# Optimization experiments

Measured on AMD Instinct MI355X. Metric: run time of the kernel, lower is better.

The kernel has to match this reference:

```python
import jax, jax.numpy as jnp
import numpy as np

B, T, V, E, U, D1, D2, C = 256, 512, 32000, 100, 512, 1024, 1024, 10
SCALE = 0.02


def setup_inputs() -> dict:
    key = jax.random.key(0)
    ks = jax.random.split(key, 12)
    return {
        "tokens": jax.random.randint(ks[0], (B, T), 0, V, dtype=jnp.int32),
        "emb": jax.random.normal(ks[1], (V, E), jnp.float32) * SCALE,
        "Wx": jax.random.normal(ks[2], (E, U), jnp.float32) * SCALE,
        "Wh": jax.random.normal(ks[3], (U, U), jnp.float32) * SCALE,
        "b_rnn": jnp.zeros((U,), jnp.float32),
        "W1": jax.random.normal(ks[4], (U, D1), jnp.float32) * SCALE,
        "b1": jnp.zeros((D1,), jnp.float32),
        "W2": jax.random.normal(ks[5], (D1, D2), jnp.float32) * SCALE,
        "b2": jnp.zeros((D2,), jnp.float32),
        "Wo": jax.random.normal(ks[6], (D2, C), jnp.float32) * SCALE,
        "bo": jnp.zeros((C,), jnp.float32),
    }


def reference(tokens, emb, Wx, Wh, b_rnn, W1, b1, W2, b2, Wo, bo):
    # Embedding with mask_zero=True: token 0 produces a masked timestep.
    x = emb[tokens]                      # [B, T, E]
    mask = tokens != 0                   # [B, T] bool

    # SimpleRNN (activation=relu, return last state). Masked steps carry state.
    xw = jnp.einsum("bte,eu->btu", x, Wx) + b_rnn  # precompute input projection [B,T,U]

    def step(h, inp):
        xw_t, m_t = inp                  # [B,U], [B]
        h_new = jax.nn.relu(xw_t + h @ Wh)
        h = jnp.where(m_t[:, None], h_new, h)
        return h, None

    h0 = jnp.zeros((tokens.shape[0], Wh.shape[0]), x.dtype)
    h_last, _ = jax.lax.scan(step, h0, (jnp.swapaxes(xw, 0, 1), mask.T))

    # MLP head: relu, relu, softmax
    h = jax.nn.relu(h_last @ W1 + b1)
    h = jax.nn.relu(h @ W2 + b2)
    return jax.nn.softmax(h @ Wo + bo, axis=-1)
```

## Files before the change

### kernel.cpp

```cpp
#include <hip/hip_runtime.h>


typedef __attribute__((ext_vector_type(8))) int i32x8_t;
typedef __attribute__((ext_vector_type(4))) float f32x4_t;

constexpr int Bn = 256, Tn = 512, En = 100, Un = 512;
constexpr int D1n = 1024, D2n = 1024, Cn = 10;
constexpr float QS  = 256.f;
constexpr float INV = 1.52587890625e-05f;
constexpr int USC = 0x7F7F7F7F;
constexpr int XW_STEP = 16 * 512 * 16;

__device__ __forceinline__ unsigned f2e4m3_sw(float x) {
    unsigned u = __float_as_uint(x);
    unsigned sgn = (u >> 24) & 0x80;
    float a = __uint_as_float(u & 0x7FFFFFFF);
    if (a >= 448.f) return sgn | 0x7E;
    if (a < 0.015625f) {
        unsigned q = (unsigned)__float2int_rn(a * 512.f);
        return sgn | q;
    }
    int e = (int)((u >> 23) & 0xFF) - 127;
    unsigned m = u & 0x7FFFFF;
    unsigned mant = m >> 20, rem = m & 0xFFFFF;
    if (rem > 0x80000 || (rem == 0x80000 && (mant & 1))) {
        if (++mant == 8) { mant = 0; ++e; }
    }
    if (e > 8) return sgn | 0x7E;
    return sgn | ((unsigned)(e + 7) << 3) | mant;
}

__device__ __forceinline__ unsigned cvt1(float x) {
#if __has_builtin(__builtin_amdgcn_cvt_pk_fp8_f32)
    return (unsigned)__builtin_amdgcn_cvt_pk_fp8_f32(x, x, 0, false) & 0xFFu;
#else
    return f2e4m3_sw(x);
#endif
}

__device__ __forceinline__ unsigned pk4(float a, float b, float c, float d) {
#if __has_builtin(__builtin_amdgcn_cvt_pk_fp8_f32)
    int r = __builtin_amdgcn_cvt_pk_fp8_f32(a, b, 0, false);
    r = __builtin_amdgcn_cvt_pk_fp8_f32(c, d, r, true);
    return (unsigned)r;
#else
    return f2e4m3_sw(a) | (f2e4m3_sw(b) << 8) | (f2e4m3_sw(c) << 16) |
           (f2e4m3_sw(d) << 24);
#endif
}

__device__ __forceinline__ ushort f2bf(float x) {
    unsigned u = __float_as_uint(x);
    unsigned r = (u + 0x7FFFu + ((u >> 16) & 1u)) >> 16;
    return (ushort)r;
}

__global__ __launch_bounds__(256) void pack_wh8(const float* __restrict__ Wh,
                                                unsigned char* __restrict__ P) {
    int e = blockIdx.x * 256 + threadIdx.x;
    int j = e & 31, l = (e >> 5) & 63, kc = (e >> 11) & 3, nt = e >> 13;
    int k = kc * 128 + (l >> 4) * 32 + j;
    int c = nt * 16 + (l & 15);
    P[e] = (unsigned char)cvt1(Wh[k * Un + c] * QS);
}

__global__ __launch_bounds__(256) void pack_wx8(const float* __restrict__ Wx,
                                                unsigned char* __restrict__ P) {
    int e = blockIdx.x * 256 + threadIdx.x;
    int j = e & 31, l = (e >> 5) & 63, nt = e >> 11;
    int k = (l >> 4) * 32 + j;
    int c = nt * 16 + (l & 15);
    P[e] = (k < En) ? (unsigned char)cvt1(Wx[k * Un + c] * QS) : 0;
}

__global__ __launch_bounds__(512) void xw_gemm(
    const int* __restrict__ tokens, const float* __restrict__ emb,
    const float* __restrict__ b_rnn, const unsigned char* __restrict__ WxP8,
    ushort* __restrict__ xwp)
{
    __shared__ char XS[32768];

    const int tid  = threadIdx.x;
    const int lane = tid & 63;
    const int wv   = tid >> 6;
    const int r0   = blockIdx.x * 16;
    const int t0   = blockIdx.y * 16;

    const int r16 = lane & 15;
    const int q   = lane >> 4;

    for (int idx = tid; idx < 6400; idx += 512) {
        int tt   = idx / 400;
        int rem  = idx - tt * 400;
        int prow = rem / 25;
        int pc4  = rem - prow * 25;
        int tok  = tokens[(r0 + prow) * Tn + t0 + tt];
        float4 v = *(const float4*)(emb + tok * En + pc4 * 4);
        *(unsigned*)(XS + tt * 2048 + ((prow * 128 + pc4 * 4) ^ (prow << 4))) =
            pk4(v.x * QS, v.y * QS, v.z * QS, v.w * QS);
    }
    for (int idx = tid; idx < 16 * 16 * 7; idx += 512) {
        int tt   = idx / 112;
        int rem  = idx - tt * 112;
        int prow = rem / 7;
        int c4   = 25 + (rem - prow * 7);
        *(unsigned*)(XS + tt * 2048 + ((prow * 128 + c4 * 4) ^ (prow << 4))) = 0;
    }
    __syncthreads();

    i32x8_t wxf[4];
#pragma unroll
    for (int p = 0; p < 4; ++p)
        wxf[p] = *(const i32x8_t*)(WxP8 + ((wv * 4 + p) * 64 + lane) * 32);

    float biasQ[4][4];
#pragma unroll
    for (int p = 0; p < 4; ++p)
#pragma unroll
        for (int j = 0; j < 4; ++j)
            biasQ[p][j] = b_rnn[(wv * 4 + p) * 16 + q * 4 + j] * 65536.f;

    const int bswz = r16 << 4;
    for (int tt = 0; tt < 16; ++tt) {
        uint4 blo = *(const uint4*)(XS + tt * 2048 +
                        ((r16 * 128 + q * 32) ^ bswz));
        uint4 bhi = *(const uint4*)(XS + tt * 2048 +
                        (((r16 * 128 + q * 32) + 16) ^ bswz));
        i32x8_t bf = {(int)blo.x, (int)blo.y, (int)blo.z, (int)blo.w,
                      (int)bhi.x, (int)bhi.y, (int)bhi.z, (int)bhi.w};
        f32x4_t acc[4];
#pragma unroll
        for (int p = 0; p < 4; ++p) {
            acc[p] = (f32x4_t){biasQ[p][0], biasQ[p][1], biasQ[p][2], biasQ[p][3]};
            acc[p] = __builtin_amdgcn_mfma_scale_f32_16x16x128_f8f6f4(
                wxf[p], bf, acc[p], 0, 0, 0, USC, 0, USC);
        }
        size_t base = (((size_t)(t0 + tt) * 16 + blockIdx.x) * 512 + tid) * 16;
        uint4 lo, hi;
        lo.x = (unsigned)f2bf(acc[0][0]) | ((unsigned)f2bf(acc[0][1]) << 16);
        lo.y = (unsigned)f2bf(acc[0][2]) | ((unsigned)f2bf(acc[0][3]) << 16);
        lo.z = (unsigned)f2bf(acc[1][0]) | ((unsigned)f2bf(acc[1][1]) << 16);
        lo.w = (unsigned)f2bf(acc[1][2]) | ((unsigned)f2bf(acc[1][3]) << 16);
        hi.x = (unsigned)f2bf(acc[2][0]) | ((unsigned)f2bf(acc[2][1]) << 16);
        hi.y = (unsigned)f2bf(acc[2][2]) | ((unsigned)f2bf(acc[2][3]) << 16);
        hi.z = (unsigned)f2bf(acc[3][0]) | ((unsigned)f2bf(acc[3][1]) << 16);
        hi.w = (unsigned)f2bf(acc[3][2]) | ((unsigned)f2bf(acc[3][3]) << 16);
        *(uint4*)(xwp + base)     = lo;
        *(uint4*)(xwp + base + 8) = hi;
    }
}

__global__ __launch_bounds__(512, 2) void rnn_persist8x(
    const int* __restrict__ tokens, const unsigned char* __restrict__ WhP8,
    const ushort* __restrict__ xwp, float* __restrict__ h_final)
{
    __shared__ char sh[32768];
    char* H0 = sh;            char* H1 = sh + 8192;
    char* TOKB = sh + 16384;

    const int tid  = threadIdx.x;
    const int lane = tid & 63;
    const int wv   = tid >> 6;
    const int r0   = blockIdx.x * 16;

    const int r16  = lane & 15;
    const int q    = lane >> 4;
    const int bswz = r16 << 4;

    for (int f = tid; f < 16 * Tn; f += 512) {
        int row = f >> 9, tt = f & 511;
        *(ushort*)(TOKB + ((((row << 10) | (tt << 1))) ^ (row << 2))) =
            (ushort)tokens[r0 * Tn + f];
    }
    {
        int* z = (int*)sh;
        for (int f = tid; f < 2048; f += 512) z[f] = 0;
    }
    __syncthreads();

    i32x8_t whf[4][4];
#pragma unroll
    for (int kc = 0; kc < 4; ++kc)
#pragma unroll
        for (int p = 0; p < 4; ++p)
            whf[kc][p] = *(const i32x8_t*)(WhP8 +
                (((wv * 4 + p) * 4 + kc) * 64 + lane) * 32);

    const ushort* xwT = xwp + ((size_t)blockIdx.x * 512 + tid) * 16;

    float hprev[4][4];
#pragma unroll
    for (int p = 0; p < 4; ++p)
#pragma unroll
        for (int j = 0; j < 4; ++j) hprev[p][j] = 0.f;

    uint4 pfA0, pfA1, pfB0, pfB1;
    pfA0 = *(const uint4*)(xwT);
    pfA1 = *(const uint4*)(xwT + 8);

#define BFL(u) __uint_as_float((u) << 16)
#define BFH(u) __uint_as_float((u) & 0xFFFF0000u)

#define RNN_STEP(T, HC, HN, C0, C1, N0, N1)                                    \
    {                                                                          \
        const int t = (T);                                                     \
        if (t + 1 < Tn) {                                                      \
            const ushort* xt = xwT + (size_t)(t + 1) * XW_STEP;                \
            N0 = *(const uint4*)(xt);                                          \
            N1 = *(const uint4*)(xt + 8);                                      \
        }                                                                      \
        f32x4_t acc[4];                                                        \
        acc[0] = (f32x4_t){BFL(C0.x), BFH(C0.x), BFL(C0.y), BFH(C0.y)};        \
        acc[1] = (f32x4_t){BFL(C0.z), BFH(C0.z), BFL(C0.w), BFH(C0.w)};        \
        acc[2] = (f32x4_t){BFL(C1.x), BFH(C1.x), BFL(C1.y), BFH(C1.y)};        \
        acc[3] = (f32x4_t){BFL(C1.z), BFH(C1.z), BFL(C1.w), BFH(C1.w)};        \
        _Pragma("unroll")                                                      \
        for (int kc = 0; kc < 4; ++kc) {                                       \
            const int bb = r16 * 512 + kc * 128 + q * 32;                      \
            uint4 blo = *(const uint4*)((HC) + ((bb) ^ bswz));                 \
            uint4 bhi = *(const uint4*)((HC) + ((bb + 16) ^ bswz));            \
            i32x8_t bf = {(int)blo.x, (int)blo.y, (int)blo.z, (int)blo.w,      \
                          (int)bhi.x, (int)bhi.y, (int)bhi.z, (int)bhi.w};     \
            _Pragma("unroll")                                                  \
            for (int p = 0; p < 4; ++p)                                        \
                acc[p] = __builtin_amdgcn_mfma_scale_f32_16x16x128_f8f6f4(     \
                    whf[kc][p], bf, acc[p], 0, 0, 0, USC, 0, USC);             \
        }                                                                      \
        const bool mk = *(const ushort*)(TOKB +                                \
            ((((r16 << 10) | (t << 1))) ^ (r16 << 2))) != 0;                   \
        _Pragma("unroll")                                                      \
        for (int p = 0; p < 4; ++p) {                                          \
            float v0 = fmaxf(acc[p][0] * INV, 0.f);                            \
            float v1 = fmaxf(acc[p][1] * INV, 0.f);                            \
            float v2 = fmaxf(acc[p][2] * INV, 0.f);                            \
            float v3 = fmaxf(acc[p][3] * INV, 0.f);                            \
            v0 = mk ? v0 : hprev[p][0];  v1 = mk ? v1 : hprev[p][1];           \
            v2 = mk ? v2 : hprev[p][2];  v3 = mk ? v3 : hprev[p][3];           \
            hprev[p][0] = v0; hprev[p][1] = v1;                                \
            hprev[p][2] = v2; hprev[p][3] = v3;                                \
            *(unsigned*)((HN) +                                                \
                ((r16 * 512 + (wv * 4 + p) * 16 + q * 4) ^ bswz)) =            \
                pk4(v0 * QS, v1 * QS, v2 * QS, v3 * QS);                       \
        }                                                                      \
        __syncthreads();                                                       \
    }

    for (int t2 = 0; t2 < Tn; t2 += 2) {
        RNN_STEP(t2,     H0, H1, pfA0, pfA1, pfB0, pfB1)
        RNN_STEP(t2 + 1, H1, H0, pfB0, pfB1, pfA0, pfA1)
    }
#undef RNN_STEP
#undef BFL
#undef BFH

#pragma unroll
    for (int p = 0; p < 4; ++p) {
        int n = (wv * 4 + p) * 16 + q * 4;
#pragma unroll
        for (int j = 0; j < 4; ++j)
            h_final[(r0 + r16) * Un + n + j] = hprev[p][j];
    }
}

__global__ __launch_bounds__(512, 2) void rnn_persist8(
    const int* __restrict__ tokens, const float* __restrict__ emb,
    const float* __restrict__ b_rnn,
    const unsigned char* __restrict__ WhP8, const unsigned char* __restrict__ WxP8,
    float* __restrict__ h_final)
{
    __shared__ char sh[36864];
    char* H0 = sh;            char* H1 = sh + 8192;
    char* X0 = sh + 16384;    char* X1 = sh + 18432;
    char* TOKB = sh + 20480;

    const int tid  = threadIdx.x;
    const int lane = tid & 63;
    const int wv   = tid >> 6;
    const int r0   = blockIdx.x * 16;

    const int r16  = lane & 15;
    const int q    = lane >> 4;
    const int bswz = r16 << 4;

    for (int f = tid; f < 16 * Tn; f += 512) {
        int row = f >> 9, tt = f & 511;
        *(ushort*)(TOKB + ((((row << 10) | (tt << 1))) ^ (row << 2))) =
            (ushort)tokens[r0 * Tn + f];
    }
    {
        int* z = (int*)sh;
        for (int f = tid; f < 2048; f += 512) z[f] = 0;
        int* zx = (int*)(sh + 16384);
        for (int f = tid; f < 1024; f += 512) zx[f] = 0;
    }
    __syncthreads();

    i32x8_t whf[4][4], wxf[4];
#pragma unroll
    for (int kc = 0; kc < 4; ++kc)
#pragma unroll
        for (int p = 0; p < 4; ++p)
            whf[kc][p] = *(const i32x8_t*)(WhP8 +
                (((wv * 4 + p) * 4 + kc) * 64 + lane) * 32);
#pragma unroll
    for (int p = 0; p < 4; ++p)
        wxf[p] = *(const i32x8_t*)(WxP8 + ((wv * 4 + p) * 64 + lane) * 32);

    float bias_r[4][4];
#pragma unroll
    for (int p = 0; p < 4; ++p)
#pragma unroll
        for (int j = 0; j < 4; ++j)
            bias_r[p][j] = b_rnn[(wv * 4 + p) * 16 + q * 4 + j];

    const int prow = tid / 25;
    const int pc4  = tid - prow * 25;
    const bool is_pref = (tid < 400);
    const int pxaddr = (prow * 128 + pc4 * 4) ^ (prow << 4);

    if (is_pref) {
        int tk = (int)*(const ushort*)(TOKB + (((prow << 10)) ^ (prow << 2)));
        float4 v = *(const float4*)(emb + tk * En + pc4 * 4);
        *(unsigned*)(X0 + pxaddr) = pk4(v.x * QS, v.y * QS, v.z * QS, v.w * QS);
    }
    __syncthreads();

    float hprev[4][4];
#pragma unroll
    for (int p = 0; p < 4; ++p)
#pragma unroll
        for (int j = 0; j < 4; ++j) hprev[p][j] = 0.f;

#define RNN_STEP(T, HC, HN, XC, XN)                                            \
    {                                                                          \
        const int t = (T);                                                     \
        float4 pref;                                                           \
        const bool dp = is_pref && (t + 1 < Tn);                               \
        if (dp) {                                                              \
            int tk = (int)*(const ushort*)(TOKB +                              \
                ((((prow << 10) | ((t + 1) << 1))) ^ (prow << 2)));            \
            pref = *(const float4*)(emb + tk * En + pc4 * 4);                  \
        }                                                                      \
        f32x4_t acc[4];                                                        \
        _Pragma("unroll")                                                      \
        for (int p = 0; p < 4; ++p) acc[p] = (f32x4_t){0.f, 0.f, 0.f, 0.f};    \
        _Pragma("unroll")                                                      \
        for (int kc = 0; kc < 4; ++kc) {                                       \
            const int bb = r16 * 512 + kc * 128 + q * 32;                      \
            uint4 blo = *(const uint4*)((HC) + ((bb) ^ bswz));                 \
            uint4 bhi = *(const uint4*)((HC) + ((bb + 16) ^ bswz));            \
            i32x8_t bf = {(int)blo.x, (int)blo.y, (int)blo.z, (int)blo.w,      \
                          (int)bhi.x, (int)bhi.y, (int)bhi.z, (int)bhi.w};     \
            _Pragma("unroll")                                                  \
            for (int p = 0; p < 4; ++p)                                        \
                acc[p] = __builtin_amdgcn_mfma_scale_f32_16x16x128_f8f6f4(     \
                    whf[kc][p], bf, acc[p], 0, 0, 0, USC, 0, USC);             \
        }                                                                      \
        {                                                                      \
            const int xb = r16 * 128 + q * 32;                                 \
            uint4 blo = *(const uint4*)((XC) + ((xb) ^ bswz));                 \
            uint4 bhi = *(const uint4*)((XC) + ((xb + 16) ^ bswz));            \
            i32x8_t bf = {(int)blo.x, (int)blo.y, (int)blo.z, (int)blo.w,      \
                          (int)bhi.x, (int)bhi.y, (int)bhi.z, (int)bhi.w};     \
            _Pragma("unroll")                                                  \
            for (int p = 0; p < 4; ++p)                                        \
                acc[p] = __builtin_amdgcn_mfma_scale_f32_16x16x128_f8f6f4(     \
                    wxf[p], bf, acc[p], 0, 0, 0, USC, 0, USC);                 \
        }                                                                      \
        const bool mk = *(const ushort*)(TOKB +                                \
            ((((r16 << 10) | (t << 1))) ^ (r16 << 2))) != 0;                   \
        _Pragma("unroll")                                                      \
        for (int p = 0; p < 4; ++p) {                                          \
            float v0 = fmaxf(acc[p][0] * INV + bias_r[p][0], 0.f);             \
            float v1 = fmaxf(acc[p][1] * INV + bias_r[p][1], 0.f);             \
            float v2 = fmaxf(acc[p][2] * INV + bias_r[p][2], 0.f);             \
            float v3 = fmaxf(acc[p][3] * INV + bias_r[p][3], 0.f);             \
            v0 = mk ? v0 : hprev[p][0];  v1 = mk ? v1 : hprev[p][1];           \
            v2 = mk ? v2 : hprev[p][2];  v3 = mk ? v3 : hprev[p][3];           \
            hprev[p][0] = v0; hprev[p][1] = v1;                                \
            hprev[p][2] = v2; hprev[p][3] = v3;                                \
            *(unsigned*)((HN) +                                                \
                ((r16 * 512 + (wv * 4 + p) * 16 + q * 4) ^ bswz)) =            \
                pk4(v0 * QS, v1 * QS, v2 * QS, v3 * QS);                       \
        }                                                                      \
        if (dp) {                                                              \
            *(unsigned*)((XN) + pxaddr) =                                      \
                pk4(pref.x * QS, pref.y * QS, pref.z * QS, pref.w * QS);       \
        }                                                                      \
        __syncthreads();                                                       \
    }

    for (int t2 = 0; t2 < Tn; t2 += 2) {
        RNN_STEP(t2,     H0, H1, X0, X1)
        RNN_STEP(t2 + 1, H1, H0, X1, X0)
    }
#undef RNN_STEP

#pragma unroll
    for (int p = 0; p < 4; ++p) {
        int n = (wv * 4 + p) * 16 + q * 4;
#pragma unroll
        for (int j = 0; j < 4; ++j)
            h_final[(r0 + r16) * Un + n + j] = hprev[p][j];
    }
}

template <int K, bool RELU>
__global__ __launch_bounds__(256) void fc32(
    const float* __restrict__ in, const float* __restrict__ W,
    const float* __restrict__ b, float* __restrict__ out, int N)
{
    __shared__ float in_lds[32][512];
    const int tid = threadIdx.x;
    const int r0  = blockIdx.y * 32;
    const int c0  = blockIdx.x * 32;

    const int col = c0 + (tid & 31);
    const int rq  = (tid >> 5) * 4;

    float acc0 = b[col], acc1 = acc0, acc2 = acc0, acc3 = acc0;

    for (int kc = 0; kc < K / 512; ++kc) {
        if (kc) __syncthreads();
        for (int i = tid; i < 32 * 512; i += 256) {
            int r = i >> 9, c = i & 511;
            in_lds[r][c] = in[(r0 + r) * K + kc * 512 + c];
        }
        __syncthreads();

        const float4* v0 = (const float4*)(&in_lds[rq + 0][0]);
        const float4* v1 = (const float4*)(&in_lds[rq + 1][0]);
        const float4* v2 = (const float4*)(&in_lds[rq + 2][0]);
        const float4* v3 = (const float4*)(&in_lds[rq + 3][0]);
        for (int k4 = 0; k4 < 128; ++k4) {
            float4 a0 = v0[k4], a1 = v1[k4], a2 = v2[k4], a3 = v3[k4];
            int k = kc * 512 + k4 * 4;
            float w0 = W[(k + 0) * N + col];
            float w1 = W[(k + 1) * N + col];
            float w2 = W[(k + 2) * N + col];
            float w3 = W[(k + 3) * N + col];
            acc0 += a0.x * w0 + a0.y * w1 + a0.z * w2 + a0.w * w3;
            acc1 += a1.x * w0 + a1.y * w1 + a1.z * w2 + a1.w * w3;
            acc2 += a2.x * w0 + a2.y * w1 + a2.z * w2 + a2.w * w3;
            acc3 += a3.x * w0 + a3.y * w1 + a3.z * w2 + a3.w * w3;
        }
    }
    if (RELU) {
        acc0 = fmaxf(acc0, 0.f); acc1 = fmaxf(acc1, 0.f);
        acc2 = fmaxf(acc2, 0.f); acc3 = fmaxf(acc3, 0.f);
    }
    out[(r0 + rq + 0) * N + col] = acc0;
    out[(r0 + rq + 1) * N + col] = acc1;
    out[(r0 + rq + 2) * N + col] = acc2;
    out[(r0 + rq + 3) * N + col] = acc3;
}

__global__ __launch_bounds__(64) void head_softmax(
    const float* __restrict__ h2, const float* __restrict__ Wo,
    const float* __restrict__ bo, float* __restrict__ out)
{
    const int b    = blockIdx.x;
    const int lane = threadIdx.x;

    float acc[Cn];
#pragma unroll
    for (int c = 0; c < Cn; ++c) acc[c] = 0.f;

    for (int k = lane; k < D2n; k += 64) {
        float hv = h2[b * D2n + k];
#pragma unroll
        for (int c = 0; c < Cn; ++c) acc[c] += hv * Wo[k * Cn + c];
    }
#pragma unroll
    for (int c = 0; c < Cn; ++c) {
#pragma unroll
        for (int off = 32; off > 0; off >>= 1)
            acc[c] += __shfl_down(acc[c], off);
    }
    if (lane == 0) {
        float l[Cn], mx = -1e30f;
#pragma unroll
        for (int c = 0; c < Cn; ++c) { l[c] = acc[c] + bo[c]; mx = fmaxf(mx, l[c]); }
        float s = 0.f;
#pragma unroll
        for (int c = 0; c < Cn; ++c) { l[c] = __expf(l[c] - mx); s += l[c]; }
        float inv = 1.f / s;
#pragma unroll
        for (int c = 0; c < Cn; ++c) out[b * Cn + c] = l[c] * inv;
    }
}

extern "C" void kernel_launch(void* const* d_in, const int* in_sizes, int n_in,
                              void* d_out, int out_size, void* d_ws, size_t ws_size,
                              hipStream_t stream)
{
    const int*   tokens = (const int*)d_in[0];
    const float* emb    = (const float*)d_in[1];
    const float* Wx     = (const float*)d_in[2];
    const float* Wh     = (const float*)d_in[3];
    const float* b_rnn  = (const float*)d_in[4];
    const float* W1     = (const float*)d_in[5];
    const float* b1     = (const float*)d_in[6];
    const float* W2     = (const float*)d_in[7];
    const float* b2     = (const float*)d_in[8];
    const float* Wo     = (const float*)d_in[9];
    const float* bo     = (const float*)d_in[10];
    float* out = (float*)d_out;

    char* ws = (char*)d_ws;
    unsigned char* WhP8 = (unsigned char*)ws;
    unsigned char* WxP8 = (unsigned char*)(ws + (256 << 10));
    float* h_last = (float*)(ws + (320 << 10));
    float* h1     = (float*)(ws + (832 << 10));
    float* h2     = (float*)(ws + (1856 << 10));
    ushort* xwp   = (ushort*)(ws + (3u << 20));
    const size_t need = (3u << 20) + (size_t)Tn * 16 * 512 * 16 * sizeof(ushort);

    pack_wh8<<<1024, 256, 0, stream>>>(Wh, WhP8);
    pack_wx8<<<256, 256, 0, stream>>>(Wx, WxP8);

    if (ws_size >= need) {
        xw_gemm<<<dim3(16, 32), 512, 0, stream>>>(tokens, emb, b_rnn, WxP8, xwp);
        rnn_persist8x<<<Bn / 16, 512, 0, stream>>>(tokens, WhP8, xwp, h_last);
    } else {
        rnn_persist8<<<Bn / 16, 512, 0, stream>>>(
            tokens, emb, b_rnn, WhP8, WxP8, h_last);
    }

    dim3 bs(256);
    fc32<Un, true><<<dim3(D1n / 32, Bn / 32), bs, 0, stream>>>(h_last, W1, b1, h1, D1n);
    fc32<D1n, true><<<dim3(D2n / 32, Bn / 32), bs, 0, stream>>>(h1, W2, b2, h2, D2n);
    head_softmax<<<Bn, 64, 0, stream>>>(h2, Wo, bo, out);
}
```

Measured before the change: 611.4 us.

## Streamline RNN step: bitmask token flags, lighter barrier, bias added post-MFMA

Each block precomputes a 32-bit per-row mask of nonzero tokens in shared memory, replacing per-step 16-bit token loads. The step barrier becomes an explicit lgkmcnt wait plus s_barrier instead of __syncthreads, and the xw prefetch no longer has a bounds branch; the buffer is enlarged by one step so the final prefetch reads padding. The precomputed xw is now stored in real units and added with an FMA after the recurrent MFMA rather than used as the accumulator seed. Shared memory per block shrinks, and bf16 rounding of xw now happens in real scale rather than in quantised scale.

```diff
diff --git a/kernel.cpp b/kernel.cpp
--- a/kernel.cpp
+++ b/kernel.cpp
@@ -55,6 +55,11 @@
     return (ushort)r;
 }
 
+__device__ __forceinline__ void lds_barrier() {
+    asm volatile("s_waitcnt lgkmcnt(0)" ::: "memory");
+    __builtin_amdgcn_s_barrier();
+}
+
 __global__ __launch_bounds__(256) void pack_wh8(const float* __restrict__ Wh,
                                                 unsigned char* __restrict__ P) {
     int e = blockIdx.x * 256 + threadIdx.x;
@@ -113,12 +118,12 @@
     for (int p = 0; p < 4; ++p)
         wxf[p] = *(const i32x8_t*)(WxP8 + ((wv * 4 + p) * 64 + lane) * 32);
 
-    float biasQ[4][4];
+    float bias_r[4][4];
 #pragma unroll
     for (int p = 0; p < 4; ++p)
 #pragma unroll
         for (int j = 0; j < 4; ++j)
-            biasQ[p][j] = b_rnn[(wv * 4 + p) * 16 + q * 4 + j] * 65536.f;
+            bias_r[p][j] = b_rnn[(wv * 4 + p) * 16 + q * 4 + j];
 
     const int bswz = r16 << 4;
     for (int tt = 0; tt < 16; ++tt) {
@@ -131,20 +136,27 @@
         f32x4_t acc[4];
 #pragma unroll
         for (int p = 0; p < 4; ++p) {
-            acc[p] = (f32x4_t){biasQ[p][0], biasQ[p][1], biasQ[p][2], biasQ[p][3]};
+            acc[p] = (f32x4_t){0.f, 0.f, 0.f, 0.f};
             acc[p] = __builtin_amdgcn_mfma_scale_f32_16x16x128_f8f6f4(
                 wxf[p], bf, acc[p], 0, 0, 0, USC, 0, USC);
         }
+        float v[4][4];
+#pragma unroll
+        for (int p = 0; p < 4; ++p)
+#pragma unroll
+            for (int j = 0; j < 4; ++j)
+                v[p][j] = fmaf(acc[p][j], INV, bias_r[p][j]);
+
         size_t base = (((size_t)(t0 + tt) * 16 + blockIdx.x) * 512 + tid) * 16;
         uint4 lo, hi;
-        lo.x = (unsigned)f2bf(acc[0][0]) | ((unsigned)f2bf(acc[0][1]) << 16);
-        lo.y = (unsigned)f2bf(acc[0][2]) | ((unsigned)f2bf(acc[0][3]) << 16);
-        lo.z = (unsigned)f2bf(acc[1][0]) | ((unsigned)f2bf(acc[1][1]) << 16);
-        lo.w = (unsigned)f2bf(acc[1][2]) | ((unsigned)f2bf(acc[1][3]) << 16);
-        hi.x = (unsigned)f2bf(acc[2][0]) | ((unsigned)f2bf(acc[2][1]) << 16);
-        hi.y = (unsigned)f2bf(acc[2][2]) | ((unsigned)f2bf(acc[2][3]) << 16);
-        hi.z = (unsigned)f2bf(acc[3][0]) | ((unsigned)f2bf(acc[3][1]) << 16);
-        hi.w = (unsigned)f2bf(acc[3][2]) | ((unsigned)f2bf(acc[3][3]) << 16);
+        lo.x = (unsigned)f2bf(v[0][0]) | ((unsigned)f2bf(v[0][1]) << 16);
+        lo.y = (unsigned)f2bf(v[0][2]) | ((unsigned)f2bf(v[0][3]) << 16);
+        lo.z = (unsigned)f2bf(v[1][0]) | ((unsigned)f2bf(v[1][1]) << 16);
+        lo.w = (unsigned)f2bf(v[1][2]) | ((unsigned)f2bf(v[1][3]) << 16);
+        hi.x = (unsigned)f2bf(v[2][0]) | ((unsigned)f2bf(v[2][1]) << 16);
+        hi.y = (unsigned)f2bf(v[2][2]) | ((unsigned)f2bf(v[2][3]) << 16);
+        hi.z = (unsigned)f2bf(v[3][0]) | ((unsigned)f2bf(v[3][1]) << 16);
+        hi.w = (unsigned)f2bf(v[3][2]) | ((unsigned)f2bf(v[3][3]) << 16);
         *(uint4*)(xwp + base)     = lo;
         *(uint4*)(xwp + base + 8) = hi;
     }
@@ -154,9 +166,9 @@
     const int* __restrict__ tokens, const unsigned char* __restrict__ WhP8,
     const ushort* __restrict__ xwp, float* __restrict__ h_final)
 {
-    __shared__ char sh[32768];
+    __shared__ char sh[17408];
     char* H0 = sh;            char* H1 = sh + 8192;
-    char* TOKB = sh + 16384;
+    unsigned* TOKM = (unsigned*)(sh + 16384);
 
     const int tid  = threadIdx.x;
     const int lane = tid & 63;
@@ -167,10 +179,13 @@
     const int q    = lane >> 4;
     const int bswz = r16 << 4;
 
-    for (int f = tid; f < 16 * Tn; f += 512) {
-        int row = f >> 9, tt = f & 511;
-        *(ushort*)(TOKB + ((((row << 10) | (tt << 1))) ^ (row << 2))) =
-            (ushort)tokens[r0 * Tn + f];
+    if (tid < 256) {
+        int row = tid >> 4, ch = tid & 15;
+        const int* tp = tokens + (r0 + row) * Tn + ch * 32;
+        unsigned m = 0;
+#pragma unroll
+        for (int i = 0; i < 32; ++i) m |= (tp[i] != 0 ? 1u : 0u) << i;
+        TOKM[row * 16 + ch] = m;
     }
     {
         int* z = (int*)sh;
@@ -187,6 +202,7 @@
                 (((wv * 4 + p) * 4 + kc) * 64 + lane) * 32);
 
     const ushort* xwT = xwp + ((size_t)blockIdx.x * 512 + tid) * 16;
+    const ushort* xnext = xwT + XW_STEP;
 
     float hprev[4][4];
 #pragma unroll
@@ -194,26 +210,21 @@
 #pragma unroll
         for (int j = 0; j < 4; ++j) hprev[p][j] = 0.f;
 
-    uint4 pfA0, pfA1, pfB0, pfB1;
-    pfA0 = *(const uint4*)(xwT);
-    pfA1 = *(const uint4*)(xwT + 8);
+    uint4 pfA0 = *(const uint4*)(xwT);
+    uint4 pfA1 = *(const uint4*)(xwT + 8);
+    uint4 pfB0, pfB1;
 
 #define BFL(u) __uint_as_float((u) << 16)
 #define BFH(u) __uint_as_float((u) & 0xFFFF0000u)
 
-#define RNN_STEP(T, HC, HN, C0, C1, N0, N1)                                    \
+#define RNN_STEP(HC, HN, C0, C1, N0, N1, MK)                                   \
     {                                                                          \
-        const int t = (T);                                                     \
-        if (t + 1 < Tn) {                                                      \
-            const ushort* xt = xwT + (size_t)(t + 1) * XW_STEP;                \
-            N0 = *(const uint4*)(xt);                                          \
-            N1 = *(const uint4*)(xt + 8);                                      \
-        }                                                                      \
+        N0 = *(const uint4*)(xnext);                                           \
+        N1 = *(const uint4*)(xnext + 8);                                       \
+        xnext += XW_STEP;                                                      \
         f32x4_t acc[4];                                                        \
-        acc[0] = (f32x4_t){BFL(C0.x), BFH(C0.x), BFL(C0.y), BFH(C0.y)};        \
-        acc[1] = (f32x4_t){BFL(C0.z), BFH(C0.z), BFL(C0.w), BFH(C0.w)};        \
-        acc[2] = (f32x4_t){BFL(C1.x), BFH(C1.x), BFL(C1.y), BFH(C1.y)};        \
-        acc[3] = (f32x4_t){BFL(C1.z), BFH(C1.z), BFL(C1.w), BFH(C1.w)};        \
+        _Pragma("unroll")                                                      \
+        for (int p = 0; p < 4; ++p) acc[p] = (f32x4_t){0.f, 0.f, 0.f, 0.f};    \
         _Pragma("unroll")                                                      \
         for (int kc = 0; kc < 4; ++kc) {                                       \
             const int bb = r16 * 512 + kc * 128 + q * 32;                      \
@@ -226,14 +237,17 @@
                 acc[p] = __builtin_amdgcn_mfma_scale_f32_16x16x128_f8f6f4(     \
                     whf[kc][p], bf, acc[p], 0, 0, 0, USC, 0, USC);             \
         }                                                                      \
-        const bool mk = *(const ushort*)(TOKB +                                \
-            ((((r16 << 10) | (t << 1))) ^ (r16 << 2))) != 0;                   \
+        const bool mk = (MK);                                                  \
         _Pragma("unroll")                                                      \
         for (int p = 0; p < 4; ++p) {                                          \
-            float v0 = fmaxf(acc[p][0] * INV, 0.f);                            \
-            float v1 = fmaxf(acc[p][1] * INV, 0.f);                            \
-            float v2 = fmaxf(acc[p][2] * INV, 0.f);                            \
-            float v3 = fmaxf(acc[p][3] * INV, 0.f);                            \
+            unsigned wlo = (p < 2) ? ((p & 1) ? C0.z : C0.x)                   \
+                                   : ((p & 1) ? C1.z : C1.x);                  \
+            unsigned whi = (p < 2) ? ((p & 1) ? C0.w : C0.y)                   \
+                                   : ((p & 1) ? C1.w : C1.y);                  \
+            float v0 = fmaxf(fmaf(acc[p][0], INV, BFL(wlo)), 0.f);             \
+            float v1 = fmaxf(fmaf(acc[p][1], INV, BFH(wlo)), 0.f);             \
+            float v2 = fmaxf(fmaf(acc[p][2], INV, BFL(whi)), 0.f);             \
+            float v3 = fmaxf(fmaf(acc[p][3], INV, BFH(whi)), 0.f);             \
             v0 = mk ? v0 : hprev[p][0];  v1 = mk ? v1 : hprev[p][1];           \
             v2 = mk ? v2 : hprev[p][2];  v3 = mk ? v3 : hprev[p][3];           \
             hprev[p][0] = v0; hprev[p][1] = v1;                                \
@@ -242,12 +256,16 @@
                 ((r16 * 512 + (wv * 4 + p) * 16 + q * 4) ^ bswz)) =            \
                 pk4(v0 * QS, v1 * QS, v2 * QS, v3 * QS);                       \
         }                                                                      \
-        __syncthreads();                                                       \
-    }
-
-    for (int t2 = 0; t2 < Tn; t2 += 2) {
-        RNN_STEP(t2,     H0, H1, pfA0, pfA1, pfB0, pfB1)
-        RNN_STEP(t2 + 1, H1, H0, pfB0, pfB1, pfA0, pfA1)
+        lds_barrier();                                                         \
+    }
+
+    const unsigned* mrow = TOKM + r16 * 16;
+    for (int tc = 0; tc < 16; ++tc) {
+        unsigned m32 = mrow[tc];
+        for (int ii = 0; ii < 16; ++ii) {
+            RNN_STEP(H0, H1, pfA0, pfA1, pfB0, pfB1, (m32 & 1u) != 0) m32 >>= 1;
+            RNN_STEP(H1, H0, pfB0, pfB1, pfA0, pfA1, (m32 & 1u) != 0) m32 >>= 1;
+        }
     }
 #undef RNN_STEP
 #undef BFL
@@ -514,7 +532,8 @@
     float* h1     = (float*)(ws + (832 << 10));
     float* h2     = (float*)(ws + (1856 << 10));
     ushort* xwp   = (ushort*)(ws + (3u << 20));
-    const size_t need = (3u << 20) + (size_t)Tn * 16 * 512 * 16 * sizeof(ushort);
+    const size_t need = (3u << 20) +
+        (size_t)(Tn + 1) * XW_STEP * sizeof(ushort);
 
     pack_wh8<<<1024, 256, 0, stream>>>(Wh, WhP8);
     pack_wx8<<<256, 256, 0, stream>>>(Wx, WxP8);
```

Result: faster. 551.9 us (-9.7%).
